# Performance work log

Measured on AMD Instinct MI355X. Metric: run time of the kernel, lower is better.

Reference implementation:

```python
import jax, jax.numpy as jnp
import numpy as np

VOCAB = 32000
EMB = 1024


def setup_inputs() -> dict:
    key = jax.random.key(0)
    k1, k2 = jax.random.split(key)
    tokens = jax.random.randint(k1, (8, 4096), 0, VOCAB, dtype=jnp.int64 if jax.config.jax_enable_x64 else jnp.int32)
    # nn.Linear(vocab, emb, bias=False) weight: [emb, vocab]
    W = jax.random.normal(k2, (EMB, VOCAB), dtype=jnp.float32) * (1.0 / np.sqrt(VOCAB))
    return {"tokens": tokens, "W": W}


def reference(tokens, W):
    # Original: one_hot(tokens, vocab) @ W.T  ==  gather columns of W
    # out[b, s, :] = W[:, tokens[b, s]]
    return W.T[tokens]  # [B, S, EMB]
```

## Files before the change

### kernel.cpp

```cpp
#include <hip/hip_runtime.h>

#define VOCAB 32000
#define EMB   1024
#define TPB   512
#define COLS  32
#define TILES (VOCAB / COLS)
#define CH    128
#define PITCH 130
#define CAP_T 256

typedef float f32x4 __attribute__((ext_vector_type(4)));

__global__ __launch_bounds__(TPB) void tok_emb_zero(int* __restrict__ cnt) {
    const int i = blockIdx.x * TPB + threadIdx.x;
    if (i < TILES) cnt[i] = 0;
}

__global__ __launch_bounds__(TPB) void tok_emb_bucket(
    const int* __restrict__ tokens, int* __restrict__ cnt,
    int* __restrict__ bucket, int n_tokens) {
    const int i4 = (blockIdx.x * TPB + threadIdx.x) * 4;
    if (i4 + 3 < n_tokens) {
        const int4 tk = *reinterpret_cast<const int4*>(&tokens[i4]);
        const int tv[4] = {tk.x, tk.y, tk.z, tk.w};
#pragma unroll
        for (int j = 0; j < 4; ++j) {
            const int tok = tv[j];
            const unsigned tile = (unsigned)tok >> 5;
            if (tile < TILES) {
                const int p = atomicAdd(&cnt[tile], 1);
                if (p < CAP_T) bucket[tile * CAP_T + p] = ((i4 + j) << 5) | (tok & 31);
            }
        }
    } else {
        for (int i = i4; i < n_tokens; ++i) {
            const int tok = tokens[i];
            const unsigned tile = (unsigned)tok >> 5;
            if (tile < TILES) {
                const int p = atomicAdd(&cnt[tile], 1);
                if (p < CAP_T) bucket[tile * CAP_T + p] = (i << 5) | (tok & 31);
            }
        }
    }
}

__global__ __launch_bounds__(TPB) void tok_emb_main(
    const float* __restrict__ W, const int* __restrict__ tokens,
    const int* __restrict__ cnt, const int* __restrict__ bucket,
    f32x4* __restrict__ out4, int n_tokens) {
    __shared__ float lds[COLS * PITCH];
    __shared__ int   list[CAP_T];
    __shared__ int   scnt;

    const int tile = blockIdx.x;
    const int v0   = tile * COLS;
    const int tid  = threadIdx.x;

    auto process = [&](int m) {
        if (m == 0) return;
        for (int c0 = 0; c0 < EMB; c0 += CH) {
            __syncthreads();
#pragma unroll
            for (int it = 0; it < (CH * COLS / 4) / TPB; ++it) {
                const int idx = tid + it * TPB;
                const int r   = idx >> 3;
                const int cc  = (idx & 7) << 2;
                const float4 v = *reinterpret_cast<const float4*>(
                    &W[(size_t)(c0 + r) * VOCAB + (size_t)(v0 + cc)]);
                lds[(cc + 0) * PITCH + r] = v.x;
                lds[(cc + 1) * PITCH + r] = v.y;
                lds[(cc + 2) * PITCH + r] = v.z;
                lds[(cc + 3) * PITCH + r] = v.w;
            }
            __syncthreads();

            const int total = m << 5;
            for (int j = tid; j < total; j += TPB) {
                const int mi = j >> 5, lane = j & 31;
                const int ent = list[mi];
                const int t   = ent >> 5, col = ent & 31;
                const float* rp = &lds[col * PITCH + (lane << 2)];
                const float2 a = *reinterpret_cast<const float2*>(rp);
                const float2 b = *reinterpret_cast<const float2*>(rp + 2);
                f32x4 o;
                o.x = a.x; o.y = a.y; o.z = b.x; o.w = b.y;
                __builtin_nontemporal_store(
                    o, &out4[(size_t)t * (EMB / 4) + (c0 >> 2) + lane]);
            }
        }
    };

    const int m_total = (bucket != nullptr) ? cnt[tile] : CAP_T + 1;
    if (m_total <= CAP_T) {
        for (int j = tid; j < m_total; j += TPB) list[j] = bucket[tile * CAP_T + j];
        __syncthreads();
        process(m_total);
    } else {
        for (int lo = 0; lo < n_tokens; lo += CAP_T) {
            const int hi = (lo + CAP_T < n_tokens) ? lo + CAP_T : n_tokens;
            __syncthreads();
            if (tid == 0) scnt = 0;
            __syncthreads();
            for (int i = lo + tid; i < hi; i += TPB) {
                const unsigned d = (unsigned)(tokens[i] - v0);
                if (d < COLS) {
                    const int p = atomicAdd(&scnt, 1);
                    list[p] = (i << 5) | (int)d;
                }
            }
            __syncthreads();
            process(scnt);
        }
    }
}

extern "C" void kernel_launch(void* const* d_in, const int* in_sizes, int n_in,
                              void* d_out, int out_size, void* d_ws, size_t ws_size,
                              hipStream_t stream) {
    const int*   tokens   = (const int*)d_in[0];
    const float* W        = (const float*)d_in[1];
    f32x4*       out4     = (f32x4*)d_out;
    const int    n_tokens = in_sizes[0];

    const size_t need = (size_t)TILES * sizeof(int)
                      + (size_t)TILES * CAP_T * sizeof(int);
    if (ws_size >= need) {
        int* cnt    = (int*)d_ws;
        int* bucket = cnt + TILES;
        tok_emb_zero<<<(TILES + TPB - 1) / TPB, TPB, 0, stream>>>(cnt);
        const int quads = (n_tokens + 3) / 4;
        tok_emb_bucket<<<(quads + TPB - 1) / TPB, TPB, 0, stream>>>(
            tokens, cnt, bucket, n_tokens);
        tok_emb_main<<<TILES, TPB, 0, stream>>>(W, tokens, cnt, bucket, out4, n_tokens);
    } else {
        tok_emb_main<<<TILES, TPB, 0, stream>>>(W, tokens, nullptr, nullptr, out4, n_tokens);
    }
}
```

Before: 61.58 us.

## Widen vocab tiles, split rows across blocks, prefetch W chunks with swizzled LDS

Each tile now covers 64 vocab columns instead of 32, and every tile is split into two blocks that each handle half of the embedding rows. Each block loads the next W chunk into registers while the current chunk is being stored out, which is a software pipeline. The LDS transpose drops the padded pitch in favour of an XOR swizzle, so the gather side can read a full 16-byte vector. The intent is better DRAM coalescing on W reads, hidden load latency and wider LDS reads, at the cost of a larger per-tile bucket capacity and more registers.

```diff
diff --git a/kernel.cpp b/kernel.cpp
--- a/kernel.cpp
+++ b/kernel.cpp
@@ -3,11 +3,12 @@
 #define VOCAB 32000
 #define EMB   1024
 #define TPB   512
-#define COLS  32
+#define COLS  64
 #define TILES (VOCAB / COLS)
 #define CH    128
-#define PITCH 130
-#define CAP_T 256
+#define NCHUNK 4
+#define RG_ROWS 512
+#define CAP_T 512
 
 typedef float f32x4 __attribute__((ext_vector_type(4)));
 
@@ -25,20 +26,18 @@
         const int tv[4] = {tk.x, tk.y, tk.z, tk.w};
 #pragma unroll
         for (int j = 0; j < 4; ++j) {
-            const int tok = tv[j];
-            const unsigned tile = (unsigned)tok >> 5;
+            const unsigned tile = (unsigned)tv[j] >> 6;
             if (tile < TILES) {
                 const int p = atomicAdd(&cnt[tile], 1);
-                if (p < CAP_T) bucket[tile * CAP_T + p] = ((i4 + j) << 5) | (tok & 31);
+                if (p < CAP_T) bucket[tile * CAP_T + p] = ((i4 + j) << 6) | (tv[j] & 63);
             }
         }
     } else {
         for (int i = i4; i < n_tokens; ++i) {
-            const int tok = tokens[i];
-            const unsigned tile = (unsigned)tok >> 5;
+            const unsigned tile = (unsigned)tokens[i] >> 6;
             if (tile < TILES) {
                 const int p = atomicAdd(&cnt[tile], 1);
-                if (p < CAP_T) bucket[tile * CAP_T + p] = (i << 5) | (tok & 31);
+                if (p < CAP_T) bucket[tile * CAP_T + p] = (i << 6) | (tokens[i] & 63);
             }
         }
     }
@@ -48,52 +47,70 @@
     const float* __restrict__ W, const int* __restrict__ tokens,
     const int* __restrict__ cnt, const int* __restrict__ bucket,
     f32x4* __restrict__ out4, int n_tokens) {
-    __shared__ float lds[COLS * PITCH];
+    __shared__ float lds[COLS * CH];
     __shared__ int   list[CAP_T];
     __shared__ int   scnt;
 
-    const int tile = blockIdx.x;
-    const int v0   = tile * COLS;
-    const int tid  = threadIdx.x;
+    const int tile  = blockIdx.x >> 1;
+    const int rg    = blockIdx.x & 1;
+    const int v0    = tile * COLS;
+    const int rbase = rg * RG_ROWS;
+    const int tid   = threadIdx.x;
+
+    const int rr  = tid >> 4;
+    const int ccg = (tid & 15) << 2;
+    const int swz = (tid & 7) << 2;
+
+    const float* wbase = W + (size_t)v0 + (size_t)ccg;
 
     auto process = [&](int m) {
         if (m == 0) return;
-        for (int c0 = 0; c0 < EMB; c0 += CH) {
-            __syncthreads();
+        f32x4 ra, rb, rc, rd;
+        auto issue = [&](int c0) {
+            const float* p = wbase + (size_t)(c0 + rr) * VOCAB;
+            ra = *reinterpret_cast<const f32x4*>(p);
+            rb = *reinterpret_cast<const f32x4*>(p + (size_t)32 * VOCAB);
+            rc = *reinterpret_cast<const f32x4*>(p + (size_t)64 * VOCAB);
+            rd = *reinterpret_cast<const f32x4*>(p + (size_t)96 * VOCAB);
+        };
+        issue(rbase);
+        for (int ch = 0; ch < NCHUNK; ++ch) {
+            const int c0 = rbase + ch * CH;
+            {
+                const int s0 = (rr +  0) ^ swz;
+                const int s1 = (rr + 32) ^ swz;
+                const int s2 = (rr + 64) ^ swz;
+                const int s3 = (rr + 96) ^ swz;
 #pragma unroll
-            for (int it = 0; it < (CH * COLS / 4) / TPB; ++it) {
-                const int idx = tid + it * TPB;
-                const int r   = idx >> 3;
-                const int cc  = (idx & 7) << 2;
-                const float4 v = *reinterpret_cast<const float4*>(
-                    &W[(size_t)(c0 + r) * VOCAB + (size_t)(v0 + cc)]);
-                lds[(cc + 0) * PITCH + r] = v.x;
-                lds[(cc + 1) * PITCH + r] = v.y;
-                lds[(cc + 2) * PITCH + r] = v.z;
-                lds[(cc + 3) * PITCH + r] = v.w;
+                for (int j = 0; j < 4; ++j) lds[(ccg + j) * CH + s0] = ra[j];
+#pragma unroll
+                for (int j = 0; j < 4; ++j) lds[(ccg + j) * CH + s1] = rb[j];
+#pragma unroll
+                for (int j = 0; j < 4; ++j) lds[(ccg + j) * CH + s2] = rc[j];
+#pragma unroll
+                for (int j = 0; j < 4; ++j) lds[(ccg + j) * CH + s3] = rd[j];
             }
             __syncthreads();
-
-            const int total = m << 5;
-            for (int j = tid; j < total; j += TPB) {
-                const int mi = j >> 5, lane = j & 31;
-                const int ent = list[mi];
-                const int t   = ent >> 5, col = ent & 31;
-                const float* rp = &lds[col * PITCH + (lane << 2)];
-                const float2 a = *reinterpret_cast<const float2*>(rp);
-                const float2 b = *reinterpret_cast<const float2*>(rp + 2);
-                f32x4 o;
-                o.x = a.x; o.y = a.y; o.z = b.x; o.w = b.y;
+            if (ch + 1 < NCHUNK) issue(rbase + (ch + 1) * CH);
+            const int nst = m << 5;
+            for (int j = tid; j < nst; j += TPB) {
+                const int ent  = list[j >> 5];
+                const int lane = j & 31;
+                const int t    = ent >> 6;
+                const int col  = ent & 63;
+                const int cp   = (col >> 2) & 7;
+                const f32x4 v  = *reinterpret_cast<const f32x4*>(
+                    lds + col * CH + ((lane ^ cp) << 2));
                 __builtin_nontemporal_store(
-                    o, &out4[(size_t)t * (EMB / 4) + (c0 >> 2) + lane]);
+                    v, &out4[(size_t)t * (EMB / 4) + (c0 >> 2) + lane]);
             }
+            __syncthreads();
         }
     };
 
     const int m_total = (bucket != nullptr) ? cnt[tile] : CAP_T + 1;
     if (m_total <= CAP_T) {
         for (int j = tid; j < m_total; j += TPB) list[j] = bucket[tile * CAP_T + j];
-        __syncthreads();
         process(m_total);
     } else {
         for (int lo = 0; lo < n_tokens; lo += CAP_T) {
@@ -105,7 +122,7 @@
                 const unsigned d = (unsigned)(tokens[i] - v0);
                 if (d < COLS) {
                     const int p = atomicAdd(&scnt, 1);
-                    list[p] = (i << 5) | (int)d;
+                    list[p] = (i << 6) | (int)d;
                 }
             }
             __syncthreads();
@@ -127,12 +144,14 @@
     if (ws_size >= need) {
         int* cnt    = (int*)d_ws;
         int* bucket = cnt + TILES;
-        tok_emb_zero<<<(TILES + TPB - 1) / TPB, TPB, 0, stream>>>(cnt);
+        tok_emb_zero<<<1, TPB, 0, stream>>>(cnt);
         const int quads = (n_tokens + 3) / 4;
         tok_emb_bucket<<<(quads + TPB - 1) / TPB, TPB, 0, stream>>>(
             tokens, cnt, bucket, n_tokens);
-        tok_emb_main<<<TILES, TPB, 0, stream>>>(W, tokens, cnt, bucket, out4, n_tokens);
+        tok_emb_main<<<TILES * 2, TPB, 0, stream>>>(
+            W, tokens, cnt, bucket, out4, n_tokens);
     } else {
-        tok_emb_main<<<TILES, TPB, 0, stream>>>(W, tokens, nullptr, nullptr, out4, n_tokens);
+        tok_emb_main<<<TILES * 2, TPB, 0, stream>>>(
+            W, tokens, nullptr, nullptr, out4, n_tokens);
     }
 }
```

Measured after the change: 65.37 us. 6.1% more time.

## Prefetch W chunks into registers and use XOR-swizzled LDS with wider reads

Applied to the files above, without the earlier changes.

The chunk size grows from 128 to 512 embedding rows, so each tile runs 2 chunks instead of 8. The next chunk's W loads are issued into registers before the current chunk's output stores, which overlaps global loads with the scatter-writes. The padded LDS layout becomes an XOR-swizzled one, so each output float4 is read with a single 16-byte LDS access instead of two 8-byte ones. In exchange, LDS use rises to 64KB per block and register pressure goes up, which may reduce occupancy.

```diff
diff --git a/kernel.cpp b/kernel.cpp
--- a/kernel.cpp
+++ b/kernel.cpp
@@ -5,8 +5,8 @@
 #define TPB   512
 #define COLS  32
 #define TILES (VOCAB / COLS)
-#define CH    128
-#define PITCH 130
+#define CH    512
+#define NCHUNK (EMB / CH)
 #define CAP_T 256
 
 typedef float f32x4 __attribute__((ext_vector_type(4)));
@@ -25,20 +25,18 @@
         const int tv[4] = {tk.x, tk.y, tk.z, tk.w};
 #pragma unroll
         for (int j = 0; j < 4; ++j) {
-            const int tok = tv[j];
-            const unsigned tile = (unsigned)tok >> 5;
+            const unsigned tile = (unsigned)tv[j] >> 5;
             if (tile < TILES) {
                 const int p = atomicAdd(&cnt[tile], 1);
-                if (p < CAP_T) bucket[tile * CAP_T + p] = ((i4 + j) << 5) | (tok & 31);
+                if (p < CAP_T) bucket[tile * CAP_T + p] = ((i4 + j) << 5) | (tv[j] & 31);
             }
         }
     } else {
         for (int i = i4; i < n_tokens; ++i) {
-            const int tok = tokens[i];
-            const unsigned tile = (unsigned)tok >> 5;
+            const unsigned tile = (unsigned)tokens[i] >> 5;
             if (tile < TILES) {
                 const int p = atomicAdd(&cnt[tile], 1);
-                if (p < CAP_T) bucket[tile * CAP_T + p] = (i << 5) | (tok & 31);
+                if (p < CAP_T) bucket[tile * CAP_T + p] = (i << 5) | (tokens[i] & 31);
             }
         }
     }
@@ -48,7 +46,7 @@
     const float* __restrict__ W, const int* __restrict__ tokens,
     const int* __restrict__ cnt, const int* __restrict__ bucket,
     f32x4* __restrict__ out4, int n_tokens) {
-    __shared__ float lds[COLS * PITCH];
+    __shared__ float lds[COLS * CH];
     __shared__ int   list[CAP_T];
     __shared__ int   scnt;
 
@@ -56,44 +54,60 @@
     const int v0   = tile * COLS;
     const int tid  = threadIdx.x;
 
+    const int cg  = tid & 7;
+    const int rb  = tid >> 3;
+    const int swz = cg << 2;
+
+    const float* wbase = W + (size_t)v0 + (size_t)(cg << 2);
+
+    f32x4 r[8];
+    auto issue = [&](int c0) {
+#pragma unroll
+        for (int k = 0; k < 8; ++k)
+            r[k] = *reinterpret_cast<const f32x4*>(
+                wbase + (size_t)(c0 + rb + (k << 6)) * VOCAB);
+    };
+    auto commit = [&]() {
+#pragma unroll
+        for (int k = 0; k < 8; ++k) {
+            const int rs = (rb + (k << 6)) ^ swz;
+#pragma unroll
+            for (int j = 0; j < 4; ++j)
+                lds[(((cg << 2) + j) << 9) + rs] = r[k][j];
+        }
+    };
+
     auto process = [&](int m) {
         if (m == 0) return;
-        for (int c0 = 0; c0 < EMB; c0 += CH) {
-            __syncthreads();
-#pragma unroll
-            for (int it = 0; it < (CH * COLS / 4) / TPB; ++it) {
-                const int idx = tid + it * TPB;
-                const int r   = idx >> 3;
-                const int cc  = (idx & 7) << 2;
-                const float4 v = *reinterpret_cast<const float4*>(
-                    &W[(size_t)(c0 + r) * VOCAB + (size_t)(v0 + cc)]);
-                lds[(cc + 0) * PITCH + r] = v.x;
-                lds[(cc + 1) * PITCH + r] = v.y;
-                lds[(cc + 2) * PITCH + r] = v.z;
-                lds[(cc + 3) * PITCH + r] = v.w;
+        issue(0);
+        commit();
+        __syncthreads();
+        for (int ch = 0; ch < NCHUNK; ++ch) {
+            if (ch + 1 < NCHUNK) issue((ch + 1) * CH);
+            const int c0  = ch * CH;
+            const int nst = m << 7;
+            for (int j = tid; j < nst; j += TPB) {
+                const int ent = list[j >> 7];
+                const int i   = j & 127;
+                const int t   = ent >> 5;
+                const int c   = ent & 31;
+                const f32x4 v = *reinterpret_cast<const f32x4*>(
+                    lds + (c << 9) + ((i << 2) ^ ((c >> 2) << 2)));
+                __builtin_nontemporal_store(
+                    v, &out4[(size_t)t * (EMB / 4) + (c0 >> 2) + i]);
             }
             __syncthreads();
-
-            const int total = m << 5;
-            for (int j = tid; j < total; j += TPB) {
-                const int mi = j >> 5, lane = j & 31;
-                const int ent = list[mi];
-                const int t   = ent >> 5, col = ent & 31;
-                const float* rp = &lds[col * PITCH + (lane << 2)];
-                const float2 a = *reinterpret_cast<const float2*>(rp);
-                const float2 b = *reinterpret_cast<const float2*>(rp + 2);
-                f32x4 o;
-                o.x = a.x; o.y = a.y; o.z = b.x; o.w = b.y;
-                __builtin_nontemporal_store(
-                    o, &out4[(size_t)t * (EMB / 4) + (c0 >> 2) + lane]);
+            if (ch + 1 < NCHUNK) {
+                commit();
+                __syncthreads();
             }
         }
     };
 
     const int m_total = (bucket != nullptr) ? cnt[tile] : CAP_T + 1;
     if (m_total <= CAP_T) {
-        for (int j = tid; j < m_total; j += TPB) list[j] = bucket[tile * CAP_T + j];
-        __syncthreads();
+        for (int j = tid; j < m_total; j += TPB)
+            list[j] = bucket[tile * CAP_T + j];
         process(m_total);
     } else {
         for (int lo = 0; lo < n_tokens; lo += CAP_T) {
@@ -131,8 +145,10 @@
         const int quads = (n_tokens + 3) / 4;
         tok_emb_bucket<<<(quads + TPB - 1) / TPB, TPB, 0, stream>>>(
             tokens, cnt, bucket, n_tokens);
-        tok_emb_main<<<TILES, TPB, 0, stream>>>(W, tokens, cnt, bucket, out4, n_tokens);
+        tok_emb_main<<<TILES, TPB, 0, stream>>>(
+            W, tokens, cnt, bucket, out4, n_tokens);
     } else {
-        tok_emb_main<<<TILES, TPB, 0, stream>>>(W, tokens, nullptr, nullptr, out4, n_tokens);
+        tok_emb_main<<<TILES, TPB, 0, stream>>>(
+            W, tokens, nullptr, nullptr, out4, n_tokens);
     }
 }
```

New measurement: 60.55 us. No clear change (-1.7%).
